# Performance work log

Measured on AMD Instinct MI355X. Metric: run time of the kernel, lower is better.

## Reference

```python
import jax, jax.numpy as jnp
import numpy as np

D_MODEL = 2048
N_HEADS = 16
D_HEAD = D_MODEL // N_HEADS  # 128
D_KV = 512
D_ROPE = 64
D_SPLIT = D_HEAD - D_ROPE  # 64
ROPE_BASE = 10000.0
EPS = 1e-5


def _rmsnorm(x, g):
    var = jnp.mean(x * x, axis=-1, keepdims=True) + EPS
    return g * (x * jax.lax.rsqrt(var))


def _rope_cache(seq):
    # theta over d_head frequencies, sliced to d_rope//2 then tiled x2 (as in source)
    half_rope = D_ROPE // 2
    theta = 1.0 / (ROPE_BASE ** (jnp.arange(0, D_HEAD, 2, dtype=jnp.float32) / D_HEAD))
    idx_theta = jnp.arange(seq, dtype=jnp.float32)[:, None] * theta[None, :]  # [seq, d_head//2]
    cos = jnp.tile(jnp.cos(idx_theta[:, :half_rope]), (1, 2))  # [seq, d_rope]
    sin = jnp.tile(jnp.sin(idx_theta[:, :half_rope]), (1, 2))
    return cos[None, :, None, :], sin[None, :, None, :]  # [1,seq,1,d_rope]


def _apply_rope(x, cos, sin):
    # NOTE: source does rot_x = cat(x.chunk(2,-1), -1) which is the identity,
    # so faithfully: x*cos + x*sin
    return x * cos + x * sin


def setup_inputs() -> dict:
    key = jax.random.key(0)
    ks = jax.random.split(key, 12)
    def w(k, i, o):
        return jax.random.normal(k, (i, o), dtype=jnp.float32) * (1.0 / np.sqrt(i))
    return {
        "x": jax.random.normal(ks[0], (2, 2048, D_MODEL), dtype=jnp.float32),
        "W_dq": w(ks[1], D_MODEL, D_KV),
        "W_uq": w(ks[2], D_KV, N_HEADS * D_SPLIT),
        "W_dkv": w(ks[3], D_MODEL, D_KV),
        "W_uk": w(ks[4], D_KV, N_HEADS * D_SPLIT),
        "W_uv": w(ks[5], D_KV, N_HEADS * D_HEAD),
        "W_qr": w(ks[6], D_KV, N_HEADS * D_ROPE),
        "W_kr": w(ks[7], D_MODEL, N_HEADS * D_ROPE),
        "g_q": jnp.ones((D_KV,), dtype=jnp.float32),
        "g_kv": jnp.ones((D_KV,), dtype=jnp.float32),
        "W_out": w(ks[8], D_MODEL, D_MODEL),
        "b_out": jnp.zeros((D_MODEL,), dtype=jnp.float32),
    }


def reference(x, W_dq, W_uq, W_dkv, W_uk, W_uv, W_qr, W_kr, g_q, g_kv, W_out, b_out):
    batch, seq, _ = x.shape
    cos, sin = _rope_cache(seq)

    c_q = _rmsnorm(x @ W_dq, g_q)                                   # [b,s,d_kv]
    q_base = (c_q @ W_uq).reshape(batch, seq, N_HEADS, D_SPLIT)
    q_rot = _apply_rope((c_q @ W_qr).reshape(batch, seq, N_HEADS, D_ROPE), cos, sin)

    c_kv = _rmsnorm(x @ W_dkv, g_kv)
    k_base = (c_kv @ W_uk).reshape(batch, seq, N_HEADS, D_SPLIT)
    k_rot = _apply_rope((x @ W_kr).reshape(batch, seq, N_HEADS, D_ROPE), cos, sin)
    v = (c_kv @ W_uv).reshape(batch, seq, N_HEADS, D_HEAD)

    q = jnp.concatenate([q_base, q_rot], axis=-1)                   # [b,s,h,d_head]
    k = jnp.concatenate([k_base, k_rot], axis=-1)

    scale = jnp.sqrt(jnp.float32(D_HEAD))
    scores = jnp.einsum('bnhd,bmhd->bhnm', q, k) / scale            # [b,h,s,s]
    causal = jnp.tril(jnp.ones((seq, seq), dtype=bool))
    scores = jnp.where(causal[None, None], scores, -jnp.inf)
    attn = jax.nn.softmax(scores, axis=-1)
    out = jnp.einsum('bhnm,bmhd->bnhd', attn, v)                    # [b,s,h,d_head]
    out = out.reshape(batch, seq, D_MODEL)
    return out @ W_out + b_out
```

## Files before the change

### kernel.cpp

```cpp
#include <hip/hip_runtime.h>
#include <hip/hip_bf16.h>
#include <cstdint>

typedef __bf16 v8bf __attribute__((ext_vector_type(8)));
typedef float  v4f  __attribute__((ext_vector_type(4)));

__device__ __forceinline__ unsigned short b16(float f) {
  union { float f; unsigned u; } v; v.f = f;
  unsigned u = v.u;
  return (unsigned short)((u + 0x7fffu + ((u >> 16) & 1u)) >> 16);
}
__device__ __forceinline__ float bf2f(unsigned short u) {
  union { unsigned u; float f; } v; v.u = ((unsigned)u) << 16; return v.f;
}

#define GLOAD_LDS16(g, l)                                                     \
  __builtin_amdgcn_global_load_lds(                                           \
      (const __attribute__((address_space(1))) void*)(g),                     \
      (__attribute__((address_space(3))) void*)(l), 16, 0, 0)

__global__ __launch_bounds__(256) void conv_bf16(const float* __restrict__ in,
                                                 unsigned short* __restrict__ out) {
  size_t idx = (size_t)blockIdx.x * 256 + threadIdx.x;
  v4f v = *(const v4f*)(in + idx * 4);
  unsigned long long p = (unsigned long long)b16(v[0]) |
                         ((unsigned long long)b16(v[1]) << 16) |
                         ((unsigned long long)b16(v[2]) << 32) |
                         ((unsigned long long)b16(v[3]) << 48);
  *(unsigned long long*)(out + idx * 4) = p;
}

__global__ void transpose_w(const float* __restrict__ in, unsigned short* __restrict__ out,
                            int C, int R) {
  __shared__ float tile[32][33];
  int c0 = blockIdx.x * 32, r0 = blockIdx.y * 32;
  int x = threadIdx.x, y = threadIdx.y;
#pragma unroll
  for (int i = 0; i < 4; ++i)
    tile[y + 8 * i][x] = in[(size_t)(r0 + y + 8 * i) * C + c0 + x];
  __syncthreads();
#pragma unroll
  for (int i = 0; i < 4; ++i)
    out[(size_t)(c0 + y + 8 * i) * R + r0 + x] = b16(tile[x][y + 8 * i]);
}

template <int MODE>
__global__ __launch_bounds__(256) void gemm_bt(const unsigned short* __restrict__ A,
                                               const unsigned short* __restrict__ BT,
                                               void* __restrict__ C0,
                                               const float* __restrict__ bias,
                                               int M, int N, int K) {
  __shared__ unsigned short As[128 * 32];
  __shared__ unsigned short Bs[128 * 32];
  const int tid = threadIdx.x;
  const int w = tid >> 6, l = tid & 63;
  const int wm = w >> 1, wn = w & 1;
  const int lg = l >> 4, lr = l & 15;
  const int nwg = gridDim.x * gridDim.y;
  const int f = blockIdx.y * gridDim.x + blockIdx.x;
  const int swz = (f & 7) * (nwg >> 3) + (f >> 3);
  const int m0 = (swz / gridDim.x) * 128, n0 = (swz % gridDim.x) * 128;

  const int srow = tid >> 2, scol = (tid & 3) * 8;
  const unsigned short* Ap0 = A  + (size_t)(m0 + srow) * K + scol;
  const unsigned short* Ap1 = A  + (size_t)(m0 + 64 + srow) * K + scol;
  const unsigned short* Bp0 = BT + (size_t)(n0 + srow) * K + scol;
  const unsigned short* Bp1 = BT + (size_t)(n0 + 64 + srow) * K + scol;
  unsigned short* Ad0 = As + tid * 8;
  unsigned short* Ad1 = As + 2048 + tid * 8;
  unsigned short* Bd0 = Bs + tid * 8;
  unsigned short* Bd1 = Bs + 2048 + tid * 8;

  v4f acc[4][4];
#pragma unroll
  for (int i = 0; i < 4; ++i)
#pragma unroll
    for (int j = 0; j < 4; ++j) acc[i][j] = (v4f){0.f, 0.f, 0.f, 0.f};

  for (int k0 = 0; k0 < K; k0 += 32) {
    GLOAD_LDS16(Ap0 + k0, Ad0);
    GLOAD_LDS16(Ap1 + k0, Ad1);
    GLOAD_LDS16(Bp0 + k0, Bd0);
    GLOAD_LDS16(Bp1 + k0, Bd1);
    __syncthreads();
    v8bf af[4], bfr[4];
#pragma unroll
    for (int mi = 0; mi < 4; ++mi)
      af[mi] = *(const v8bf*)&As[(wm * 64 + mi * 16 + lr) * 32 + lg * 8];
#pragma unroll
    for (int ni = 0; ni < 4; ++ni)
      bfr[ni] = *(const v8bf*)&Bs[(wn * 64 + ni * 16 + lr) * 32 + lg * 8];
#pragma unroll
    for (int mi = 0; mi < 4; ++mi)
#pragma unroll
      for (int ni = 0; ni < 4; ++ni)
        acc[mi][ni] = __builtin_amdgcn_mfma_f32_16x16x32_bf16(af[mi], bfr[ni], acc[mi][ni], 0, 0, 0);
    __syncthreads();
  }
#pragma unroll
  for (int mi = 0; mi < 4; ++mi)
#pragma unroll
    for (int ni = 0; ni < 4; ++ni) {
      const int col = n0 + wn * 64 + ni * 16 + lr;
#pragma unroll
      for (int rr = 0; rr < 4; ++rr) {
        const int row = m0 + wm * 64 + mi * 16 + lg * 4 + rr;
        const float v = acc[mi][ni][rr];
        if (MODE == 0) {
          ((float*)C0)[(size_t)row * N + col] = v + bias[col];
        } else {
          ((unsigned short*)C0)[(size_t)row * N + col] = b16(v);
        }
      }
    }
}

__global__ __launch_bounds__(256) void gemm23(const unsigned short* __restrict__ cq,
                                              const unsigned short* __restrict__ ckv,
                                              const unsigned short* __restrict__ W2T,
                                              const unsigned short* __restrict__ W3T,
                                              unsigned short* __restrict__ Qb,
                                              unsigned short* __restrict__ Kb,
                                              unsigned short* __restrict__ VT) {
  __shared__ unsigned short As[128 * 32];
  __shared__ unsigned short Bs[128 * 32];
  const int tid = threadIdx.x;
  const int w = tid >> 6, l = tid & 63;
  const int wm = w >> 1, wn = w & 1;
  const int lg = l >> 4, lr = l & 15;
  const int f = blockIdx.x;
  const int swz = (f & 7) * 160 + (f >> 3);
  const bool is3 = swz >= 512;
  const int t = is3 ? swz - 512 : swz;
  const int gx = is3 ? 24 : 16;
  const int m0 = (t / gx) * 128, n0 = (t % gx) * 128;
  const unsigned short* A  = is3 ? ckv : cq;
  const unsigned short* BT = is3 ? W3T : W2T;
  const int K = 512;

  const int srow = tid >> 2, scol = (tid & 3) * 8;
  const unsigned short* Ap0 = A  + (size_t)(m0 + srow) * K + scol;
  const unsigned short* Ap1 = A  + (size_t)(m0 + 64 + srow) * K + scol;
  const unsigned short* Bp0 = BT + (size_t)(n0 + srow) * K + scol;
  const unsigned short* Bp1 = BT + (size_t)(n0 + 64 + srow) * K + scol;
  unsigned short* Ad0 = As + tid * 8;
  unsigned short* Ad1 = As + 2048 + tid * 8;
  unsigned short* Bd0 = Bs + tid * 8;
  unsigned short* Bd1 = Bs + 2048 + tid * 8;

  v4f acc[4][4];
#pragma unroll
  for (int i = 0; i < 4; ++i)
#pragma unroll
    for (int j = 0; j < 4; ++j) acc[i][j] = (v4f){0.f, 0.f, 0.f, 0.f};

  for (int k0 = 0; k0 < K; k0 += 32) {
    GLOAD_LDS16(Ap0 + k0, Ad0);
    GLOAD_LDS16(Ap1 + k0, Ad1);
    GLOAD_LDS16(Bp0 + k0, Bd0);
    GLOAD_LDS16(Bp1 + k0, Bd1);
    __syncthreads();
    v8bf af[4], bfr[4];
#pragma unroll
    for (int mi = 0; mi < 4; ++mi)
      af[mi] = *(const v8bf*)&As[(wm * 64 + mi * 16 + lr) * 32 + lg * 8];
#pragma unroll
    for (int ni = 0; ni < 4; ++ni)
      bfr[ni] = *(const v8bf*)&Bs[(wn * 64 + ni * 16 + lr) * 32 + lg * 8];
#pragma unroll
    for (int mi = 0; mi < 4; ++mi)
#pragma unroll
      for (int ni = 0; ni < 4; ++ni)
        acc[mi][ni] = __builtin_amdgcn_mfma_f32_16x16x32_bf16(af[mi], bfr[ni], acc[mi][ni], 0, 0, 0);
    __syncthreads();
  }

#pragma unroll
  for (int mi = 0; mi < 4; ++mi)
#pragma unroll
    for (int ni = 0; ni < 4; ++ni) {
      const int col = n0 + wn * 64 + ni * 16 + lr;
      const int row0 = m0 + wm * 64 + mi * 16 + lg * 4;
      if (!is3) {
        if (col < 1024) {
          int qc = (col >> 6) * 128 + (col & 63);
#pragma unroll
          for (int rr = 0; rr < 4; ++rr)
            Qb[(size_t)(row0 + rr) * 2048 + qc] = b16(acc[mi][ni][rr]);
        } else {
          int cc = col - 1024, d = cc & 63;
          int qc = (cc >> 6) * 128 + 64 + d;
#pragma unroll
          for (int rr = 0; rr < 4; ++rr) {
            int s = (row0 + rr) & 2047;
            float ang = (float)s * __expf(-(float)(d & 31) * 0.14391156831f);
            float sn, cs; __sincosf(ang, &sn, &cs);
            Qb[(size_t)(row0 + rr) * 2048 + qc] = b16(acc[mi][ni][rr] * (cs + sn));
          }
        }
      } else {
        if (col < 1024) {
          int kc = (col >> 6) * 128 + (col & 63);
#pragma unroll
          for (int rr = 0; rr < 4; ++rr)
            Kb[(size_t)(row0 + rr) * 2048 + kc] = b16(acc[mi][ni][rr]);
        } else {
          int hd = col - 1024, h = hd >> 7, d = hd & 127;
          int b = row0 >> 11, s = row0 & 2047;
          unsigned long long p =
              (unsigned long long)b16(acc[mi][ni][0]) |
              ((unsigned long long)b16(acc[mi][ni][1]) << 16) |
              ((unsigned long long)b16(acc[mi][ni][2]) << 32) |
              ((unsigned long long)b16(acc[mi][ni][3]) << 48);
          *(unsigned long long*)&VT[(size_t)((b * 16 + h) * 128 + d) * 2048 + s] = p;
        }
      }
    }
}

__global__ __launch_bounds__(256) void rmsnorm_rope(const unsigned short* __restrict__ T1,
                                                    const float* __restrict__ gq,
                                                    const float* __restrict__ gkv,
                                                    unsigned short* __restrict__ cq,
                                                    unsigned short* __restrict__ ckv,
                                                    unsigned short* __restrict__ Kb) {
  const int row = blockIdx.x;
  const int t = threadIdx.x;
  const int s = row & 2047;
  const unsigned short* rp = T1 + (size_t)row * 2048;
  float xq0 = bf2f(rp[t]), xq1 = bf2f(rp[256 + t]);
  float xk0 = bf2f(rp[512 + t]), xk1 = bf2f(rp[768 + t]);
  float sq = xq0 * xq0 + xq1 * xq1;
  float sk = xk0 * xk0 + xk1 * xk1;
#pragma unroll
  for (int o = 1; o < 64; o <<= 1) { sq += __shfl_xor(sq, o); sk += __shfl_xor(sk, o); }
  __shared__ float red[8];
  if ((t & 63) == 0) { red[t >> 6] = sq; red[4 + (t >> 6)] = sk; }
  __syncthreads();
  float rq = rsqrtf((red[0] + red[1] + red[2] + red[3]) * (1.f / 512.f) + 1e-5f);
  float rk = rsqrtf((red[4] + red[5] + red[6] + red[7]) * (1.f / 512.f) + 1e-5f);
  cq[(size_t)row * 512 + t]        = b16(gq[t] * xq0 * rq);
  cq[(size_t)row * 512 + 256 + t]  = b16(gq[256 + t] * xq1 * rq);
  ckv[(size_t)row * 512 + t]       = b16(gkv[t] * xk0 * rk);
  ckv[(size_t)row * 512 + 256 + t] = b16(gkv[256 + t] * xk1 * rk);
#pragma unroll
  for (int i = 0; i < 4; ++i) {
    int j = t + 256 * i;
    int hh = j >> 6, d = j & 63;
    float ang = (float)s * __expf(-(float)(d & 31) * 0.14391156831f);
    float sn, cs; __sincosf(ang, &sn, &cs);
    Kb[(size_t)row * 2048 + hh * 128 + 64 + d] = b16(bf2f(rp[1024 + j]) * (cs + sn));
  }
}

__global__ __launch_bounds__(256) void flash_attn(const unsigned short* __restrict__ Qb,
                                                  const unsigned short* __restrict__ Kb,
                                                  const unsigned short* __restrict__ VTb,
                                                  unsigned short* __restrict__ Ob) {
  __shared__ unsigned short Ks[64 * 128];
  __shared__ unsigned short Vs[128 * 64];
  __shared__ unsigned short Ps[4 * 16 * 72];
  const int b = blockIdx.z, h = blockIdx.y;
  const int pj = blockIdx.x;
  const int tid = threadIdx.x;
  const int w = tid >> 6, l = tid & 63;
  const int lg = l >> 4, lr = l & 15;
  const float scale = 0.0883883476483184f;

  const unsigned short* Kbase = Kb + (size_t)b * 2048 * 2048 + h * 128;
  const unsigned short* Vbase = VTb + (size_t)(b * 16 + h) * 128 * 2048;

  for (int pass = 0; pass < 2; ++pass) {
    const int q0 = (pass ? (31 - pj) : pj) * 64;
    const int qw0 = q0 + w * 16;

    v8bf qf[4];
    {
      const unsigned short* qp = Qb + (size_t)(b * 2048 + qw0 + lr) * 2048 + h * 128 + lg * 8;
#pragma unroll
      for (int ds = 0; ds < 4; ++ds) qf[ds] = *(const v8bf*)(qp + ds * 32);
    }
    v4f oacc[8];
#pragma unroll
    for (int i = 0; i < 8; ++i) oacc[i] = (v4f){0, 0, 0, 0};
    float mrow[4] = {-1e30f, -1e30f, -1e30f, -1e30f};
    float lsum[4] = {0, 0, 0, 0};

    const int nkv = q0 + 64;
    for (int kv0 = 0; kv0 < nkv; kv0 += 64) {
#pragma unroll
      for (int i = 0; i < 4; ++i) {
        int c = tid + 256 * i;
        int r = c >> 4, dbl = c & 15;
        int off = (r * 256 + dbl * 16) ^ ((r & 7) << 4);
        *(v4f*)((char*)Ks + off) =
            *(const v4f*)(Kbase + (size_t)(kv0 + r) * 2048 + dbl * 8);
      }
#pragma unroll
      for (int i = 0; i < 4; ++i) {
        int c = tid + 256 * i;
        int d = c >> 3, kbl = c & 7;
        int off = (d * 128 + kbl * 16) ^ ((d & 7) << 4);
        *(v4f*)((char*)Vs + off) =
            *(const v4f*)(Vbase + (size_t)d * 2048 + kv0 + kbl * 8);
      }
      __syncthreads();
      {
        float st[4][4];
        __builtin_amdgcn_s_setprio(1);
#pragma unroll
        for (int kt = 0; kt < 4; ++kt) {
          v4f sacc = (v4f){0, 0, 0, 0};
          int krow = kt * 16 + lr;
#pragma unroll
          for (int ds = 0; ds < 4; ++ds) {
            int off = (krow * 256 + ds * 64 + lg * 16) ^ ((krow & 7) << 4);
            v8bf kfr = *(const v8bf*)((char*)Ks + off);
            sacc = __builtin_amdgcn_mfma_f32_16x16x32_bf16(qf[ds], kfr, sacc, 0, 0, 0);
          }
          int colk = kv0 + kt * 16 + lr;
#pragma unroll
          for (int r = 0; r < 4; ++r) {
            int qrow = qw0 + lg * 4 + r;
            st[kt][r] = (colk <= qrow) ? sacc[r] * scale : -1e30f;
          }
        }
        __builtin_amdgcn_s_setprio(0);
#pragma unroll
        for (int r = 0; r < 4; ++r) {
          float mx = fmaxf(fmaxf(st[0][r], st[1][r]), fmaxf(st[2][r], st[3][r]));
#pragma unroll
          for (int o = 1; o < 16; o <<= 1) mx = fmaxf(mx, __shfl_xor(mx, o));
          float mnew = fmaxf(mrow[r], mx);
          float sc = __expf(mrow[r] - mnew);
          float ps = 0.f;
#pragma unroll
          for (int kt = 0; kt < 4; ++kt) {
            float p = __expf(st[kt][r] - mnew);
            ps += p;
            Ps[w * 1152 + (lg * 4 + r) * 72 + kt * 16 + lr] = b16(p);
          }
          lsum[r] = lsum[r] * sc + ps;
          mrow[r] = mnew;
#pragma unroll
          for (int dt = 0; dt < 8; ++dt) oacc[dt][r] *= sc;
        }
        __builtin_amdgcn_s_setprio(1);
#pragma unroll
        for (int kh = 0; kh < 2; ++kh) {
          v8bf pa = *(const v8bf*)((char*)Ps + w * 2304 + lr * 144 + kh * 64 + lg * 16);
#pragma unroll
          for (int dt = 0; dt < 8; ++dt) {
            int d = dt * 16 + lr;
            int off = (d * 128 + kh * 64 + lg * 16) ^ ((d & 7) << 4);
            v8bf vfr = *(const v8bf*)((char*)Vs + off);
            oacc[dt] = __builtin_amdgcn_mfma_f32_16x16x32_bf16(pa, vfr, oacc[dt], 0, 0, 0);
          }
        }
        __builtin_amdgcn_s_setprio(0);
      }
      __syncthreads();
    }
#pragma unroll
    for (int r = 0; r < 4; ++r) {
      float ls = lsum[r];
#pragma unroll
      for (int o = 1; o < 16; o <<= 1) ls += __shfl_xor(ls, o);
      float inv = 1.f / ls;
      size_t orow = (size_t)(b * 2048 + qw0 + lg * 4 + r) * 2048 + h * 128;
#pragma unroll
      for (int dt = 0; dt < 8; ++dt)
        Ob[orow + dt * 16 + lr] = b16(oacc[dt][r] * inv);
    }
  }
}

extern "C" void kernel_launch(void* const* d_in, const int* in_sizes, int n_in,
                              void* d_out, int out_size, void* d_ws, size_t ws_size,
                              hipStream_t stream) {
  const float* x    = (const float*)d_in[0];
  const float* Wdq  = (const float*)d_in[1];
  const float* Wuq  = (const float*)d_in[2];
  const float* Wdkv = (const float*)d_in[3];
  const float* Wuk  = (const float*)d_in[4];
  const float* Wuv  = (const float*)d_in[5];
  const float* Wqr  = (const float*)d_in[6];
  const float* Wkr  = (const float*)d_in[7];
  const float* gq   = (const float*)d_in[8];
  const float* gkv  = (const float*)d_in[9];
  const float* Wout = (const float*)d_in[10];
  const float* bout = (const float*)d_in[11];
  float* out = (float*)d_out;

  const size_t M1 = 1024 * 1024;
  unsigned short* xb  = (unsigned short*)d_ws;
  unsigned short* Qb  = xb;
  unsigned short* T   = xb + 8 * M1;
  unsigned short* Ob  = T;
  unsigned short* W1T = xb + 20 * M1;
  unsigned short* W2T = xb + 24 * M1;
  unsigned short* W3T = xb + 25 * M1;
  unsigned short* WoT = W3T + 1536 * 1024;
  unsigned short* cq  = xb + 30 * M1 + 512 * 1024;
  unsigned short* ckv = cq + 2 * M1;
  unsigned short* Kb = (unsigned short*)d_out;
  unsigned short* VT = Kb + 8 * M1;

  dim3 b256(256), tb(32, 8);

  conv_bf16<<<8192, b256, 0, stream>>>(x, xb);
  transpose_w<<<dim3(16, 64), tb, 0, stream>>>(Wdq,  W1T,                       512, 2048);
  transpose_w<<<dim3(16, 64), tb, 0, stream>>>(Wdkv, W1T + (size_t)512 * 2048,  512, 2048);
  transpose_w<<<dim3(32, 64), tb, 0, stream>>>(Wkr,  W1T + (size_t)1024 * 2048, 1024, 2048);
  transpose_w<<<dim3(32, 16), tb, 0, stream>>>(Wuq,  W2T,                       1024, 512);
  transpose_w<<<dim3(32, 16), tb, 0, stream>>>(Wqr,  W2T + (size_t)1024 * 512,  1024, 512);
  transpose_w<<<dim3(32, 16), tb, 0, stream>>>(Wuk,  W3T,                       1024, 512);
  transpose_w<<<dim3(64, 16), tb, 0, stream>>>(Wuv,  W3T + (size_t)1024 * 512,  2048, 512);
  transpose_w<<<dim3(64, 64), tb, 0, stream>>>(Wout, WoT,                       2048, 2048);

  gemm_bt<1><<<dim3(16, 32), b256, 0, stream>>>(xb, W1T, T, nullptr, 4096, 2048, 2048);
  rmsnorm_rope<<<4096, b256, 0, stream>>>(T, gq, gkv, cq, ckv, Kb);
  gemm23<<<dim3(1280), b256, 0, stream>>>(cq, ckv, W2T, W3T, Qb, Kb, VT);

  flash_attn<<<dim3(16, 16, 2), b256, 0, stream>>>(Qb, Kb, VT, Ob);

  gemm_bt<0><<<dim3(16, 32), b256, 0, stream>>>(Ob, WoT, out, bout, 4096, 2048, 2048);
}
```

Measured before the change: 280.8 us.

## Merge prep kernels into one launch and use direct global-to-LDS loads in attention

Nine preprocessing launches (the x bf16 conversion and eight weight transposes) are merged into a single prep kernel that dispatches on block index. This cuts per-launch overhead and the gaps between launches. The flash attention K/V tile loads now use global_load_lds, writing straight into LDS and skipping the register round-trip. The XOR swizzle moves onto the global source address instead of the LDS destination, and a wrong swizzle mapping would corrupt results.

New measurement: 264.5 us. 1.06x faster.

```diff
diff --git a/kernel.cpp b/kernel.cpp
--- a/kernel.cpp
+++ b/kernel.cpp
@@ -19,29 +19,52 @@
       (const __attribute__((address_space(1))) void*)(g),                     \
       (__attribute__((address_space(3))) void*)(l), 16, 0, 0)
 
-__global__ __launch_bounds__(256) void conv_bf16(const float* __restrict__ in,
-                                                 unsigned short* __restrict__ out) {
-  size_t idx = (size_t)blockIdx.x * 256 + threadIdx.x;
-  v4f v = *(const v4f*)(in + idx * 4);
-  unsigned long long p = (unsigned long long)b16(v[0]) |
-                         ((unsigned long long)b16(v[1]) << 16) |
-                         ((unsigned long long)b16(v[2]) << 32) |
-                         ((unsigned long long)b16(v[3]) << 48);
-  *(unsigned long long*)(out + idx * 4) = p;
-}
-
-__global__ void transpose_w(const float* __restrict__ in, unsigned short* __restrict__ out,
-                            int C, int R) {
+__global__ __launch_bounds__(256) void prep(const float* __restrict__ x,
+                                            unsigned short* __restrict__ xb,
+                                            const float* __restrict__ Wdq,
+                                            const float* __restrict__ Wdkv,
+                                            const float* __restrict__ Wkr,
+                                            const float* __restrict__ Wuq,
+                                            const float* __restrict__ Wqr,
+                                            const float* __restrict__ Wuk,
+                                            const float* __restrict__ Wuv,
+                                            const float* __restrict__ Wout,
+                                            unsigned short* __restrict__ W1T,
+                                            unsigned short* __restrict__ W2T,
+                                            unsigned short* __restrict__ W3T,
+                                            unsigned short* __restrict__ WoT) {
+  const int tid = threadIdx.x;
+  int bid = blockIdx.x;
+  if (bid < 8192) {
+    size_t idx = (size_t)bid * 256 + tid;
+    v4f v = *(const v4f*)(x + idx * 4);
+    unsigned long long p = (unsigned long long)b16(v[0]) |
+                           ((unsigned long long)b16(v[1]) << 16) |
+                           ((unsigned long long)b16(v[2]) << 32) |
+                           ((unsigned long long)b16(v[3]) << 48);
+    *(unsigned long long*)(xb + idx * 4) = p;
+    return;
+  }
   __shared__ float tile[32][33];
-  int c0 = blockIdx.x * 32, r0 = blockIdx.y * 32;
-  int x = threadIdx.x, y = threadIdx.y;
+  bid -= 8192;
+  const float* in; unsigned short* out; int C, R, gx;
+  if (bid < 1024)      { in = Wdq;  out = W1T;                        C = 512;  R = 2048; gx = 16; }
+  else if (bid < 2048) { in = Wdkv; out = W1T + (size_t)512 * 2048;   C = 512;  R = 2048; gx = 16; bid -= 1024; }
+  else if (bid < 4096) { in = Wkr;  out = W1T + (size_t)1024 * 2048;  C = 1024; R = 2048; gx = 32; bid -= 2048; }
+  else if (bid < 4608) { in = Wuq;  out = W2T;                        C = 1024; R = 512;  gx = 32; bid -= 4096; }
+  else if (bid < 5120) { in = Wqr;  out = W2T + (size_t)1024 * 512;   C = 1024; R = 512;  gx = 32; bid -= 4608; }
+  else if (bid < 5632) { in = Wuk;  out = W3T;                        C = 1024; R = 512;  gx = 32; bid -= 5120; }
+  else if (bid < 6656) { in = Wuv;  out = W3T + (size_t)1024 * 512;   C = 2048; R = 512;  gx = 64; bid -= 5632; }
+  else                 { in = Wout; out = WoT;                        C = 2048; R = 2048; gx = 64; bid -= 6656; }
+  const int c0 = (bid % gx) * 32, r0 = (bid / gx) * 32;
+  const int xx = tid & 31, yy = tid >> 5;
 #pragma unroll
   for (int i = 0; i < 4; ++i)
-    tile[y + 8 * i][x] = in[(size_t)(r0 + y + 8 * i) * C + c0 + x];
+    tile[yy + 8 * i][xx] = in[(size_t)(r0 + yy + 8 * i) * C + c0 + xx];
   __syncthreads();
 #pragma unroll
   for (int i = 0; i < 4; ++i)
-    out[(size_t)(c0 + y + 8 * i) * R + r0 + x] = b16(tile[x][y + 8 * i]);
+    out[(size_t)(c0 + yy + 8 * i) * R + r0 + xx] = b16(tile[xx][yy + 8 * i]);
 }
 
 template <int MODE>
@@ -291,18 +314,14 @@
 #pragma unroll
       for (int i = 0; i < 4; ++i) {
         int c = tid + 256 * i;
-        int r = c >> 4, dbl = c & 15;
-        int off = (r * 256 + dbl * 16) ^ ((r & 7) << 4);
-        *(v4f*)((char*)Ks + off) =
-            *(const v4f*)(Kbase + (size_t)(kv0 + r) * 2048 + dbl * 8);
+        int r = c >> 4, dbl = (c & 15) ^ (r & 7);
+        GLOAD_LDS16(Kbase + (size_t)(kv0 + r) * 2048 + dbl * 8, Ks + c * 8);
       }
 #pragma unroll
       for (int i = 0; i < 4; ++i) {
         int c = tid + 256 * i;
-        int d = c >> 3, kbl = c & 7;
-        int off = (d * 128 + kbl * 16) ^ ((d & 7) << 4);
-        *(v4f*)((char*)Vs + off) =
-            *(const v4f*)(Vbase + (size_t)d * 2048 + kv0 + kbl * 8);
+        int d = c >> 3, kbl = (c & 7) ^ ((c >> 3) & 7);
+        GLOAD_LDS16(Vbase + (size_t)d * 2048 + kv0 + kbl * 8, Vs + c * 8);
       }
       __syncthreads();
       {
@@ -406,17 +425,10 @@
   unsigned short* Kb = (unsigned short*)d_out;
   unsigned short* VT = Kb + 8 * M1;
 
-  dim3 b256(256), tb(32, 8);
-
-  conv_bf16<<<8192, b256, 0, stream>>>(x, xb);
-  transpose_w<<<dim3(16, 64), tb, 0, stream>>>(Wdq,  W1T,                       512, 2048);
-  transpose_w<<<dim3(16, 64), tb, 0, stream>>>(Wdkv, W1T + (size_t)512 * 2048,  512, 2048);
-  transpose_w<<<dim3(32, 64), tb, 0, stream>>>(Wkr,  W1T + (size_t)1024 * 2048, 1024, 2048);
-  transpose_w<<<dim3(32, 16), tb, 0, stream>>>(Wuq,  W2T,                       1024, 512);
-  transpose_w<<<dim3(32, 16), tb, 0, stream>>>(Wqr,  W2T + (size_t)1024 * 512,  1024, 512);
-  transpose_w<<<dim3(32, 16), tb, 0, stream>>>(Wuk,  W3T,                       1024, 512);
-  transpose_w<<<dim3(64, 16), tb, 0, stream>>>(Wuv,  W3T + (size_t)1024 * 512,  2048, 512);
-  transpose_w<<<dim3(64, 64), tb, 0, stream>>>(Wout, WoT,                       2048, 2048);
+  dim3 b256(256);
+
+  prep<<<dim3(18944), b256, 0, stream>>>(x, xb, Wdq, Wdkv, Wkr, Wuq, Wqr, Wuk, Wuv, Wout,
+                                         W1T, W2T, W3T, WoT);
 
   gemm_bt<1><<<dim3(16, 32), b256, 0, stream>>>(xb, W1T, T, nullptr, 4096, 2048, 2048);
   rmsnorm_rope<<<4096, b256, 0, stream>>>(T, gq, gkv, cq, ckv, Kb);
```
